# Kernel tuning notes

Hardware: AMD Instinct MI355X
Metric: run time of the kernel (lower is better)

The kernel has to match this reference:

```python
import jax, jax.numpy as jnp
import numpy as np

N_NODES = 10000
N_EDGES = 320000
NODE_C = 256
IN_EDGE_C = 256
OUT_EDGE_C = 512
BN_EPS = 1e-5


def setup_inputs() -> dict:
    key = jax.random.key(0)
    ks = jax.random.split(key, 10)
    d_in = 2 * NODE_C + IN_EDGE_C  # 768
    x = jax.random.normal(ks[0], (N_NODES, NODE_C), dtype=jnp.float32)
    edge_index = jax.random.randint(ks[1], (2, N_EDGES), 0, N_NODES, dtype=jnp.int64)
    edge_attr = jax.random.normal(ks[2], (N_EDGES, IN_EDGE_C), dtype=jnp.float32)
    # MLP params (Linear stored as [in, out] for x @ W + b)
    W1 = jax.random.normal(ks[3], (d_in, OUT_EDGE_C), dtype=jnp.float32) / np.sqrt(d_in)
    b1 = jnp.zeros((OUT_EDGE_C,), dtype=jnp.float32)
    W2 = jax.random.normal(ks[4], (OUT_EDGE_C, OUT_EDGE_C), dtype=jnp.float32) / np.sqrt(OUT_EDGE_C)
    b2 = jnp.zeros((OUT_EDGE_C,), dtype=jnp.float32)
    # BatchNorm affine params
    gamma = jnp.ones((OUT_EDGE_C,), dtype=jnp.float32)
    beta = jnp.zeros((OUT_EDGE_C,), dtype=jnp.float32)
    return {"x": x, "edge_index": edge_index, "edge_attr": edge_attr,
            "W1": W1, "b1": b1, "W2": W2, "b2": b2,
            "gamma": gamma, "beta": beta}


def reference(x, edge_index, edge_attr, W1, b1, W2, b2, gamma, beta):
    src = edge_index[0]  # x_j (source / neighbor)
    dst = edge_index[1]  # x_i (target, aggregation index)
    x_i = x[dst]                                  # [E, node_c]
    x_j = x[src]                                  # [E, node_c]
    m = jnp.concatenate([x_i, x_j - x_i, edge_attr], axis=-1)  # [E, 2*node_c+edge_c]
    h = jax.nn.relu(m @ W1 + b1) @ W2 + b2        # per-edge MLP -> [E, out_c]
    out = jax.ops.segment_sum(h, dst, num_segments=x.shape[0])  # scatter-add -> [N, out_c]
    # BatchNorm1d (training-mode batch statistics, biased variance)
    mean = jnp.mean(out, axis=0)
    var = jnp.var(out, axis=0)
    y = (out - mean) * jax.lax.rsqrt(var + BN_EPS) * gamma + beta
    return jax.nn.relu(y)
```

## Files before the change

kernel.cpp:

```cpp
#include <hip/hip_runtime.h>
#include <hip/hip_bf16.h>
#include <cstdint>

#define NN 10000
#define NE 320000
#define NC 256
#define OC 512
#define K1 256

typedef __bf16 bf16_t;
typedef bf16_t bf16x8 __attribute__((ext_vector_type(8)));
typedef bf16_t bf16x4 __attribute__((ext_vector_type(4)));
typedef float  f32x4  __attribute__((ext_vector_type(4)));

__device__ __forceinline__ void gload_lds16(const void* g, void* l) {
  __builtin_amdgcn_global_load_lds(
      (const __attribute__((address_space(1))) unsigned int*)g,
      (__attribute__((address_space(3))) unsigned int*)l, 16, 0, 0);
}

__device__ __forceinline__ int permB(int R) {
  return (R & ~63) + ((R & 15) << 2) + ((R >> 4) & 3);
}

__global__ void k_prep(const float* __restrict__ x,
                       const float* __restrict__ W1,
                       const float* __restrict__ W2,
                       bf16_t* __restrict__ xb,
                       bf16_t* __restrict__ w1abt,
                       bf16_t* __restrict__ w1ct,
                       bf16_t* __restrict__ w2t,
                       float* __restrict__ agg,
                       int* __restrict__ deg,
                       int* __restrict__ cursor,
                       float* __restrict__ sums) {
  const int stride = gridDim.x * blockDim.x;
  for (int i = blockIdx.x * blockDim.x + threadIdx.x; i < NN * OC; i += stride) {
    agg[i] = 0.0f;
    if (i < NN * NC) xb[i] = (bf16_t)x[i];
    if (i < 1024 * K1) {
      const int n = i >> 8, k = i & 255;
      float w;
      if (n < OC) w = W1[(size_t)k * OC + n] - W1[(size_t)(k + NC) * OC + n];
      else        w = W1[(size_t)(k + NC) * OC + (n - OC)];
      w1abt[i] = (bf16_t)w;
    }
    if (i < OC * K1) {
      const int n = i >> 8, k = i & 255;
      w1ct[i] = (bf16_t)W1[(size_t)(512 + k) * OC + n];
    }
    if (i < OC * OC) {
      const int n = i >> 9, k = i & 511;
      w2t[i] = (bf16_t)W2[(size_t)k * OC + n];
    }
    if (i < NN) { deg[i] = 0; cursor[i] = 0; }
    if (i < 1024) sums[i] = 0.0f;
  }
}

__global__ void k_deg(const int* __restrict__ dstIdx, int* __restrict__ deg) {
  const int i = blockIdx.x * blockDim.x + threadIdx.x;
  if (i < NE) atomicAdd(&deg[dstIdx[i]], 1);
}

__global__ void k_scan(const int* __restrict__ deg, int* __restrict__ offs) {
  __shared__ int carry;
  __shared__ int wsum[4];
  if (threadIdx.x == 0) carry = 0;
  __syncthreads();
  const int lane = threadIdx.x & 63, w = threadIdx.x >> 6;
  for (int base = 0; base < NN; base += 256) {
    const int i = base + threadIdx.x;
    const int v = (i < NN) ? deg[i] : 0;
    int s = v;
#pragma unroll
    for (int d = 1; d < 64; d <<= 1) { int t = __shfl_up(s, d); if (lane >= d) s += t; }
    if (lane == 63) wsum[w] = s;
    __syncthreads();
    int woff = 0;
    for (int j = 0; j < w; j++) woff += wsum[j];
    const int incl = s + woff + carry;
    if (i < NN) offs[i] = incl - v;
    __syncthreads();
    if (threadIdx.x == 255) carry = incl;
    __syncthreads();
  }
}

__global__ void k_scatter(const int* __restrict__ srcIdx, const int* __restrict__ dstIdx,
                          const int* __restrict__ offs, int* __restrict__ cursor,
                          int* __restrict__ eperm, int* __restrict__ sdst,
                          int* __restrict__ ssrc) {
  const int e = blockIdx.x * blockDim.x + threadIdx.x;
  if (e < NE) {
    const int d = dstIdx[e];
    const int pos = offs[d] + atomicAdd(&cursor[d], 1);
    eperm[pos] = e;
    sdst[pos] = d;
    ssrc[pos] = srcIdx[e];
  }
}

__global__ __launch_bounds__(256) void k_pq(
    const bf16_t* __restrict__ xb,
    const bf16_t* __restrict__ w1abt,
    const float*  __restrict__ b1,
    float*        __restrict__ P,
    bf16_t*       __restrict__ Qb) {
  __shared__ bf16_t sA[128 * 64];
  __shared__ bf16_t sB[128 * 64];

  const int tid = threadIdx.x;
  const int cb = blockIdx.x & 7, rblk = blockIdx.x >> 3;
  const int r0 = rblk * 128, n0 = cb * 128;
  const int lane = tid & 63, wid = tid >> 6;
  const int mbase = (wid >> 1) * 64, nbase = (wid & 1) * 64;
  const int lr = lane >> 3, ls = lane & 7, slog = ls ^ lr;
  const int g = lane >> 4;

  f32x4 acc[4][4];
#pragma unroll
  for (int mi = 0; mi < 4; mi++)
#pragma unroll
    for (int ni = 0; ni < 4; ni++) acc[mi][ni] = (f32x4){0.f, 0.f, 0.f, 0.f};

  for (int kb = 0; kb < K1; kb += 64) {
#pragma unroll
    for (int i = 0; i < 4; i++) {
      const int row = wid * 32 + i * 8;
      int grow = r0 + row + lr;
      if (grow > NN - 1) grow = NN - 1;
      gload_lds16(xb + (size_t)grow * NC + kb + slog * 8, &sA[row * 64]);
      gload_lds16(w1abt + (size_t)(n0 + permB(row + lr)) * K1 + kb + slog * 8,
                  &sB[row * 64]);
    }
    __syncthreads();
#pragma unroll
    for (int kk = 0; kk < 2; kk++) {
      const int sl = kk * 4 + g;
      bf16x8 av[4], bv[4];
#pragma unroll
      for (int mi = 0; mi < 4; mi++) {
        const int rA = mbase + mi * 16 + (lane & 15);
        av[mi] = *(const bf16x8*)&sA[rA * 64 + ((sl ^ (rA & 7)) * 8)];
      }
#pragma unroll
      for (int ni = 0; ni < 4; ni++) {
        const int rB = nbase + ni * 16 + (lane & 15);
        bv[ni] = *(const bf16x8*)&sB[rB * 64 + ((sl ^ (rB & 7)) * 8)];
      }
#pragma unroll
      for (int mi = 0; mi < 4; mi++)
#pragma unroll
        for (int ni = 0; ni < 4; ni++)
          acc[mi][ni] = __builtin_amdgcn_mfma_f32_16x16x32_bf16(av[mi], bv[ni], acc[mi][ni], 0, 0, 0);
    }
    __syncthreads();
  }

  const int col0 = n0 + nbase + (lane & 15) * 4;
  f32x4 b1v = {0.f, 0.f, 0.f, 0.f};
  if (col0 < OC) b1v = *(const f32x4*)&b1[col0];
#pragma unroll
  for (int mi = 0; mi < 4; mi++) {
#pragma unroll
    for (int q = 0; q < 4; q++) {
      const int grow = r0 + mbase + mi * 16 + g * 4 + q;
      if (grow < NN) {
        if (col0 < OC) {
          f32x4 v;
#pragma unroll
          for (int j = 0; j < 4; j++) v[j] = acc[mi][j][q] + b1v[j];
          *(f32x4*)&P[(size_t)grow * OC + col0] = v;
        } else {
          bf16x4 v;
#pragma unroll
          for (int j = 0; j < 4; j++) v[j] = (bf16_t)acc[mi][j][q];
          *(bf16x4*)&Qb[(size_t)grow * OC + (col0 - OC)] = v;
        }
      }
    }
  }
}

__global__ __launch_bounds__(256, 2) void k_edge_gemm(
    const float*  __restrict__ ea,
    const bf16_t* __restrict__ w1ct,
    const float*  __restrict__ P,
    const bf16_t* __restrict__ Qb,
    const int*    __restrict__ eperm,
    const int*    __restrict__ sdst,
    const int*    __restrict__ ssrc,
    float*        __restrict__ agg) {
  __shared__ bf16_t sM[2][128 * 64];
  __shared__ bf16_t sW[2][128 * 64];
  __shared__ int sDst[128];
  __shared__ int sSrc[128];
  __shared__ int sE[128];

  const int bid = (blockIdx.x & 7) * 1250 + (blockIdx.x >> 3);
  const int cb = bid & 3, eblk = bid >> 2;
  const int e0 = eblk * 128, n0 = cb * 128;

  const int tid = threadIdx.x;
  if (tid < 128) {
    sDst[tid] = sdst[e0 + tid];
    sSrc[tid] = ssrc[e0 + tid];
    sE[tid]   = eperm[e0 + tid];
  }
  __syncthreads();

  const int lane = tid & 63, wid = tid >> 6;
  const int mbase = (wid >> 1) * 64, nbase = (wid & 1) * 64;
  const int g = lane >> 4, r = lane & 15;
  const int lr = lane >> 3, ls = lane & 7, slogW = ls ^ lr;
  const int mrow = tid >> 1, qd = tid & 1;
  const int msw = mrow & 7;
  const float* eaRow = ea + (size_t)sE[mrow] * NC;

#define STAGE_W(kt, b)                                                        \
  _Pragma("unroll") for (int i = 0; i < 4; i++) {                             \
    const int rowb = wid * 32 + i * 8;                                        \
    gload_lds16(w1ct + (size_t)(n0 + permB(rowb + lr)) * K1 + (kt)*64 + slogW * 8, \
                &sW[b][rowb * 64]);                                           \
  }
#define LOAD_A(kt)                                                            \
  _Pragma("unroll") for (int j = 0; j < 8; j++)                               \
      a[j] = *(const f32x4*)(eaRow + (kt)*64 + qd * 32 + j * 4);
#define WRITE_M(b)                                                            \
  _Pragma("unroll") for (int tt = 0; tt < 4; tt++) {                          \
    const int slot = qd * 4 + tt;                                             \
    bf16x8 v;                                                                 \
    _Pragma("unroll") for (int jj = 0; jj < 4; jj++) {                        \
      v[jj] = (bf16_t)a[tt * 2][jj];                                          \
      v[4 + jj] = (bf16_t)a[tt * 2 + 1][jj];                                  \
    }                                                                         \
    *(bf16x8*)&sM[b][mrow * 64 + ((slot ^ msw) * 8)] = v;                     \
  }

  f32x4 a[8];
  STAGE_W(0, 0);
  LOAD_A(0);

  const int col0 = n0 + nbase + r * 4;
  f32x4  Pp[4][4];
  bf16x4 Qp[4][4];
#pragma unroll
  for (int mi = 0; mi < 4; mi++) {
    const int rbase = mbase + mi * 16 + g * 4;
#pragma unroll
    for (int q = 0; q < 4; q++) {
      Pp[mi][q] = *(const f32x4*)&P[(size_t)sDst[rbase + q] * OC + col0];
      Qp[mi][q] = *(const bf16x4*)&Qb[(size_t)sSrc[rbase + q] * OC + col0];
    }
  }

  WRITE_M(0);

  f32x4 acc[4][4];
#pragma unroll
  for (int mi = 0; mi < 4; mi++)
#pragma unroll
    for (int ni = 0; ni < 4; ni++) acc[mi][ni] = (f32x4){0.f, 0.f, 0.f, 0.f};

#pragma unroll
  for (int t = 0; t < 4; t++) {
    const int b = t & 1;
    __syncthreads();
    if (t < 3) { STAGE_W(t + 1, b ^ 1); LOAD_A(t + 1); }
#pragma unroll
    for (int kk = 0; kk < 2; kk++) {
      const int sl = kk * 4 + g;
      bf16x8 av[4], bv[4];
#pragma unroll
      for (int mi = 0; mi < 4; mi++) {
        const int rA = mbase + mi * 16 + r;
        av[mi] = *(const bf16x8*)&sM[b][rA * 64 + ((sl ^ (rA & 7)) * 8)];
      }
#pragma unroll
      for (int ni = 0; ni < 4; ni++) {
        const int rB = nbase + ni * 16 + r;
        bv[ni] = *(const bf16x8*)&sW[b][rB * 64 + ((sl ^ (rB & 7)) * 8)];
      }
#pragma unroll
      for (int mi = 0; mi < 4; mi++)
#pragma unroll
        for (int ni = 0; ni < 4; ni++)
          acc[mi][ni] = __builtin_amdgcn_mfma_f32_16x16x32_bf16(av[mi], bv[ni], acc[mi][ni], 0, 0, 0);
    }
    if (t < 3) { WRITE_M(b ^ 1); }
  }
#undef STAGE_W
#undef LOAD_A
#undef WRITE_M

#pragma unroll
  for (int mi = 0; mi < 4; mi++) {
    const int rbase = mbase + mi * 16 + g * 4;
    const int d0 = sDst[rbase],     d1 = sDst[rbase + 1];
    const int d2 = sDst[rbase + 2], d3 = sDst[rbase + 3];
    const int headId = d0, tailId = d3;
    const bool b1q = (d1 != d0), b2q = (d2 != d1), b3q = (d3 != d2);
    const bool seen = b1q | b2q | b3q;
    bool match[3];
#pragma unroll
    for (int j = 0; j < 3; j++) {
      const int tIdj = __shfl(tailId, (lane & 15) | (j << 4));
      match[j] = (j < g) && (tIdj == headId);
    }
    const int nextHead = __shfl(headId, (lane + 16) & 63);
    const bool endsHere = (g == 3) || (nextHead != tailId);

    f32x4 v0, v1, v2, v3;
#pragma unroll
    for (int j = 0; j < 4; j++) {
      v0[j] = fmaxf(acc[mi][j][0] + Pp[mi][0][j] + (float)Qp[mi][0][j], 0.f);
      v1[j] = fmaxf(acc[mi][j][1] + Pp[mi][1][j] + (float)Qp[mi][1][j], 0.f);
      v2[j] = fmaxf(acc[mi][j][2] + Pp[mi][2][j] + (float)Qp[mi][2][j], 0.f);
      v3[j] = fmaxf(acc[mi][j][3] + Pp[mi][3][j] + (float)Qp[mi][3][j], 0.f);
    }

    f32x4 head = {0.f, 0.f, 0.f, 0.f}, run = v0;
    bool first = true;
    if (b1q) { head = run; first = false; run = v1; } else run += v1;
    if (b2q) {
      if (first) { head = run; first = false; }
      else {
        float* base = agg + (size_t)d1 * OC + col0;
#pragma unroll
        for (int j = 0; j < 4; j++) if (run[j] != 0.f) atomicAdd(base + j, run[j]);
      }
      run = v2;
    } else run += v2;
    if (b3q) {
      if (first) { head = run; first = false; }
      else {
        float* base = agg + (size_t)d2 * OC + col0;
#pragma unroll
        for (int j = 0; j < 4; j++) if (run[j] != 0.f) atomicAdd(base + j, run[j]);
      }
      run = v3;
    } else run += v3;
    const f32x4 tailSum = run;

    f32x4 inc = {0.f, 0.f, 0.f, 0.f};
#pragma unroll
    for (int jg = 0; jg < 3; jg++) {
      f32x4 ts;
#pragma unroll
      for (int c = 0; c < 4; c++) ts[c] = __shfl(tailSum[c], (lane & 15) | (jg << 4));
      if (match[jg]) inc += ts;
    }
    if (seen) {
      float* base = agg + (size_t)headId * OC + col0;
#pragma unroll
      for (int j = 0; j < 4; j++) {
        const float h = head[j] + inc[j];
        if (h != 0.f) atomicAdd(base + j, h);
      }
    }
    if (endsHere) {
      float* base = agg + (size_t)tailId * OC + col0;
#pragma unroll
      for (int j = 0; j < 4; j++) {
        const float t2 = tailSum[j] + (seen ? 0.f : inc[j]);
        if (t2 != 0.f) atomicAdd(base + j, t2);
      }
    }
  }
}

__global__ __launch_bounds__(256) void k_node_gemm(
    const float*  __restrict__ agg,
    const bf16_t* __restrict__ w2t,
    const float*  __restrict__ b2,
    const int*    __restrict__ deg,
    float*        __restrict__ out,
    float*        __restrict__ sums) {
  __shared__ bf16_t sM[128 * 72];
  __shared__ bf16_t sW[128 * 72];

  const int tid  = threadIdx.x;
  const int bid  = blockIdx.x;
  const int cb   = bid & 3;
  const int rblk = bid >> 2;
  const int r0   = rblk * 128;
  const int n0   = cb * 128;

  const int lane  = tid & 63, wid = tid >> 6;
  const int mbase = (wid >> 1) * 64, nbase = (wid & 1) * 64;
  const int se = tid >> 1;
  const int sk = (tid & 1) * 32;
  const int arow  = r0 + se;
  const bool rowok = arow < NN;

  f32x4 acc[4][4];
#pragma unroll
  for (int mi = 0; mi < 4; mi++)
#pragma unroll
    for (int ni = 0; ni < 4; ni++) acc[mi][ni] = (f32x4){0.f, 0.f, 0.f, 0.f};

  for (int kb = 0; kb < OC; kb += 64) {
    {
      bf16x8* dst = (bf16x8*)&sM[se * 72 + sk];
      if (rowok) {
        const float* pf = agg + (size_t)arow * OC + kb + sk;
        f32x4 f[8];
#pragma unroll
        for (int i = 0; i < 8; i++) f[i] = *(const f32x4*)(pf + i * 4);
#pragma unroll
        for (int i = 0; i < 4; i++) {
          bf16x8 v;
#pragma unroll
          for (int j = 0; j < 4; j++) {
            v[j]     = (bf16_t)f[2 * i][j];
            v[4 + j] = (bf16_t)f[2 * i + 1][j];
          }
          dst[i] = v;
        }
      } else {
        bf16x8 z = {};
        dst[0] = z; dst[1] = z; dst[2] = z; dst[3] = z;
      }
    }
    {
      const bf16_t* pw = w2t + (size_t)(n0 + permB(se)) * OC + kb + sk;
      bf16x8* dst = (bf16x8*)&sW[se * 72 + sk];
      dst[0] = *(const bf16x8*)(pw);
      dst[1] = *(const bf16x8*)(pw + 8);
      dst[2] = *(const bf16x8*)(pw + 16);
      dst[3] = *(const bf16x8*)(pw + 24);
    }
    __syncthreads();
#pragma unroll
    for (int kk = 0; kk < 2; kk++) {
      const int krd = kk * 32 + (lane >> 4) * 8;
      bf16x8 av[4], bv[4];
#pragma unroll
      for (int mi = 0; mi < 4; mi++)
        av[mi] = *(const bf16x8*)&sM[(mbase + mi * 16 + (lane & 15)) * 72 + krd];
#pragma unroll
      for (int ni = 0; ni < 4; ni++)
        bv[ni] = *(const bf16x8*)&sW[(nbase + ni * 16 + (lane & 15)) * 72 + krd];
#pragma unroll
      for (int mi = 0; mi < 4; mi++)
#pragma unroll
        for (int ni = 0; ni < 4; ni++)
          acc[mi][ni] = __builtin_amdgcn_mfma_f32_16x16x32_bf16(av[mi], bv[ni], acc[mi][ni], 0, 0, 0);
    }
    __syncthreads();
  }

  const int col0 = n0 + nbase + (lane & 15) * 4;
  const f32x4 b2v = *(const f32x4*)&b2[col0];
  const int g = lane >> 4;
  f32x4 s1 = {0.f, 0.f, 0.f, 0.f}, s2 = {0.f, 0.f, 0.f, 0.f};
#pragma unroll
  for (int mi = 0; mi < 4; mi++) {
#pragma unroll
    for (int q = 0; q < 4; q++) {
      const int row = r0 + mbase + mi * 16 + g * 4 + q;
      if (row < NN) {
        const float dg = (float)deg[row];
        f32x4 v;
#pragma unroll
        for (int j = 0; j < 4; j++) {
          v[j] = acc[mi][j][q] + b2v[j] * dg;
          s1[j] += v[j];
          s2[j] += v[j] * v[j];
        }
        *(f32x4*)&out[(size_t)row * OC + col0] = v;
      }
    }
  }
#pragma unroll
  for (int j = 0; j < 4; j++) {
    s1[j] += __shfl_xor(s1[j], 16);  s2[j] += __shfl_xor(s2[j], 16);
    s1[j] += __shfl_xor(s1[j], 32);  s2[j] += __shfl_xor(s2[j], 32);
  }
  if (g == 0) {
#pragma unroll
    for (int j = 0; j < 4; j++) {
      atomicAdd(&sums[col0 + j], s1[j]);
      atomicAdd(&sums[OC + col0 + j], s2[j]);
    }
  }
}

__global__ void k_bn_apply(float* __restrict__ out,
                           const float* __restrict__ sums,
                           const float* __restrict__ gamma,
                           const float* __restrict__ beta) {
  const int i = blockIdx.x * blockDim.x + threadIdx.x;
  f32x4 v = *((const f32x4*)out + i);
  const int c = (i & 127) << 2;
  const f32x4 sm = *(const f32x4*)&sums[c];
  const f32x4 sq = *(const f32x4*)&sums[OC + c];
  const f32x4 gm = *(const f32x4*)&gamma[c];
  const f32x4 bt = *(const f32x4*)&beta[c];
  f32x4 r;
#pragma unroll
  for (int j = 0; j < 4; j++) {
    const float mean = sm[j] * (1.0f / NN);
    const float var  = sq[j] * (1.0f / NN) - mean * mean;
    const float sc   = rsqrtf(var + 1e-5f) * gm[j];
    r[j] = fmaxf(v[j] * sc + (bt[j] - mean * sc), 0.0f);
  }
  *((f32x4*)out + i) = r;
}

extern "C" void kernel_launch(void* const* d_in, const int* in_sizes, int n_in,
                              void* d_out, int out_size, void* d_ws, size_t ws_size,
                              hipStream_t stream) {
  const float* x     = (const float*)d_in[0];
  const int*   ei    = (const int*)d_in[1];
  const float* ea    = (const float*)d_in[2];
  const float* W1    = (const float*)d_in[3];
  const float* b1    = (const float*)d_in[4];
  const float* W2    = (const float*)d_in[5];
  const float* b2    = (const float*)d_in[6];
  const float* gamma = (const float*)d_in[7];
  const float* beta  = (const float*)d_in[8];
  float* out = (float*)d_out;

  char* ws = (char*)d_ws;
  float*  agg    = (float*)(ws);
  float*  P      = (float*)(ws + 20480000);
  bf16_t* Qb     = (bf16_t*)(ws + 40960000);
  bf16_t* xb     = (bf16_t*)(ws + 51200000);
  bf16_t* w1abt  = (bf16_t*)(ws + 56320000);
  bf16_t* w1ct   = (bf16_t*)(ws + 56844288);
  bf16_t* w2t    = (bf16_t*)(ws + 57106432);
  int*    deg    = (int*)(ws + 57630720);
  int*    offs   = (int*)(ws + 57670720);
  int*    cursor = (int*)(ws + 57710720);
  float*  sums   = (float*)(ws + 57750720);
  int*    eperm  = (int*)(ws + 57754816);
  int*    sdst   = (int*)(ws + 59034816);
  int*    ssrc   = (int*)(ws + 60314816);

  const int* srcIdx = ei;
  const int* dstIdx = ei + NE;

  k_prep<<<4096, 256, 0, stream>>>(x, W1, W2, xb, w1abt, w1ct, w2t, agg, deg, cursor, sums);
  k_deg<<<(NE + 255) / 256, 256, 0, stream>>>(dstIdx, deg);
  k_scan<<<1, 256, 0, stream>>>(deg, offs);
  k_scatter<<<(NE + 255) / 256, 256, 0, stream>>>(srcIdx, dstIdx, offs, cursor,
                                                  eperm, sdst, ssrc);
  k_pq<<<((NN + 127) / 128) * 8, 256, 0, stream>>>(xb, w1abt, b1, P, Qb);
  k_edge_gemm<<<(NE / 128) * 4, 256, 0, stream>>>(ea, w1ct, P, Qb, eperm, sdst, ssrc, agg);
  k_node_gemm<<<((NN + 127) / 128) * 4, 256, 0, stream>>>(agg, w2t, b2, deg, out, sums);
  k_bn_apply<<<(NN * OC / 4 + 255) / 256, 256, 0, stream>>>(out, sums, gamma, beta);
}
```

Baseline: 500.3 us.

## Split edge GEMM block into eight waves with narrower column tiles

The edge GEMM block grows from 256 to 512 threads, and each wave now covers a 64x32 output tile instead of 64x64. The ea-row staging and W-tile loads are redistributed across the extra threads, using a new column permutation that matches the two-column-per-lane epilogue. The P/Q gathers move from before the K loop into the epilogue, which cuts accumulator and prefetch register pressure so more waves can be resident. In exchange, the gather latency is no longer hidden behind the MFMA loop, and the loads become narrower 8-byte/4-byte accesses.

```diff
diff --git a/kernel.cpp b/kernel.cpp
--- a/kernel.cpp
+++ b/kernel.cpp
@@ -11,7 +11,9 @@
 typedef __bf16 bf16_t;
 typedef bf16_t bf16x8 __attribute__((ext_vector_type(8)));
 typedef bf16_t bf16x4 __attribute__((ext_vector_type(4)));
+typedef bf16_t bf16x2 __attribute__((ext_vector_type(2)));
 typedef float  f32x4  __attribute__((ext_vector_type(4)));
+typedef float  f32x2  __attribute__((ext_vector_type(2)));
 
 __device__ __forceinline__ void gload_lds16(const void* g, void* l) {
   __builtin_amdgcn_global_load_lds(
@@ -21,6 +23,9 @@
 
 __device__ __forceinline__ int permB(int R) {
   return (R & ~63) + ((R & 15) << 2) + ((R >> 4) & 3);
+}
+__device__ __forceinline__ int permB32(int R) {
+  return (R & ~31) + ((R & 15) << 1) + ((R >> 4) & 1);
 }
 
 __global__ void k_prep(const float* __restrict__ x,
@@ -183,7 +188,7 @@
   }
 }
 
-__global__ __launch_bounds__(256, 2) void k_edge_gemm(
+__global__ __launch_bounds__(512, 4) void k_edge_gemm(
     const float*  __restrict__ ea,
     const bf16_t* __restrict__ w1ct,
     const float*  __restrict__ P,
@@ -211,25 +216,26 @@
   __syncthreads();
 
   const int lane = tid & 63, wid = tid >> 6;
-  const int mbase = (wid >> 1) * 64, nbase = (wid & 1) * 64;
+  const int mbase = (wid >> 2) * 64;
+  const int nbase = (wid & 3) * 32;
   const int g = lane >> 4, r = lane & 15;
   const int lr = lane >> 3, ls = lane & 7, slogW = ls ^ lr;
-  const int mrow = tid >> 1, qd = tid & 1;
+  const int mrow = tid >> 2, qd = tid & 3;
   const int msw = mrow & 7;
   const float* eaRow = ea + (size_t)sE[mrow] * NC;
 
 #define STAGE_W(kt, b)                                                        \
-  _Pragma("unroll") for (int i = 0; i < 4; i++) {                             \
-    const int rowb = wid * 32 + i * 8;                                        \
-    gload_lds16(w1ct + (size_t)(n0 + permB(rowb + lr)) * K1 + (kt)*64 + slogW * 8, \
+  _Pragma("unroll") for (int i = 0; i < 2; i++) {                             \
+    const int rowb = wid * 16 + i * 8;       \
+    gload_lds16(w1ct + (size_t)(n0 + permB32(rowb + lr)) * K1 + (kt)*64 + slogW * 8, \
                 &sW[b][rowb * 64]);                                           \
   }
 #define LOAD_A(kt)                                                            \
-  _Pragma("unroll") for (int j = 0; j < 8; j++)                               \
-      a[j] = *(const f32x4*)(eaRow + (kt)*64 + qd * 32 + j * 4);
+  _Pragma("unroll") for (int j = 0; j < 4; j++)                               \
+      a[j] = *(const f32x4*)(eaRow + (kt)*64 + qd * 16 + j * 4);
 #define WRITE_M(b)                                                            \
-  _Pragma("unroll") for (int tt = 0; tt < 4; tt++) {                          \
-    const int slot = qd * 4 + tt;                                             \
+  _Pragma("unroll") for (int tt = 0; tt < 2; tt++) {                          \
+    const int slot = qd * 2 + tt;                                             \
     bf16x8 v;                                                                 \
     _Pragma("unroll") for (int jj = 0; jj < 4; jj++) {                        \
       v[jj] = (bf16_t)a[tt * 2][jj];                                          \
@@ -238,30 +244,16 @@
     *(bf16x8*)&sM[b][mrow * 64 + ((slot ^ msw) * 8)] = v;                     \
   }
 
-  f32x4 a[8];
+  f32x4 a[4];
   STAGE_W(0, 0);
   LOAD_A(0);
-
-  const int col0 = n0 + nbase + r * 4;
-  f32x4  Pp[4][4];
-  bf16x4 Qp[4][4];
-#pragma unroll
-  for (int mi = 0; mi < 4; mi++) {
-    const int rbase = mbase + mi * 16 + g * 4;
-#pragma unroll
-    for (int q = 0; q < 4; q++) {
-      Pp[mi][q] = *(const f32x4*)&P[(size_t)sDst[rbase + q] * OC + col0];
-      Qp[mi][q] = *(const bf16x4*)&Qb[(size_t)sSrc[rbase + q] * OC + col0];
-    }
-  }
-
   WRITE_M(0);
 
-  f32x4 acc[4][4];
+  f32x4 acc[4][2];
 #pragma unroll
   for (int mi = 0; mi < 4; mi++)
 #pragma unroll
-    for (int ni = 0; ni < 4; ni++) acc[mi][ni] = (f32x4){0.f, 0.f, 0.f, 0.f};
+    for (int ni = 0; ni < 2; ni++) acc[mi][ni] = (f32x4){0.f, 0.f, 0.f, 0.f};
 
 #pragma unroll
   for (int t = 0; t < 4; t++) {
@@ -271,21 +263,21 @@
 #pragma unroll
     for (int kk = 0; kk < 2; kk++) {
       const int sl = kk * 4 + g;
-      bf16x8 av[4], bv[4];
+      bf16x8 av[4], bv[2];
 #pragma unroll
       for (int mi = 0; mi < 4; mi++) {
         const int rA = mbase + mi * 16 + r;
         av[mi] = *(const bf16x8*)&sM[b][rA * 64 + ((sl ^ (rA & 7)) * 8)];
       }
 #pragma unroll
-      for (int ni = 0; ni < 4; ni++) {
+      for (int ni = 0; ni < 2; ni++) {
         const int rB = nbase + ni * 16 + r;
         bv[ni] = *(const bf16x8*)&sW[b][rB * 64 + ((sl ^ (rB & 7)) * 8)];
       }
 #pragma unroll
       for (int mi = 0; mi < 4; mi++)
 #pragma unroll
-        for (int ni = 0; ni < 4; ni++)
+        for (int ni = 0; ni < 2; ni++)
           acc[mi][ni] = __builtin_amdgcn_mfma_f32_16x16x32_bf16(av[mi], bv[ni], acc[mi][ni], 0, 0, 0);
     }
     if (t < 3) { WRITE_M(b ^ 1); }
@@ -294,11 +286,14 @@
 #undef LOAD_A
 #undef WRITE_M
 
+  const int col0 = n0 + nbase + r * 2;
 #pragma unroll
   for (int mi = 0; mi < 4; mi++) {
     const int rbase = mbase + mi * 16 + g * 4;
     const int d0 = sDst[rbase],     d1 = sDst[rbase + 1];
     const int d2 = sDst[rbase + 2], d3 = sDst[rbase + 3];
+    const int s0 = sSrc[rbase],     s1 = sSrc[rbase + 1];
+    const int s2 = sSrc[rbase + 2], s3 = sSrc[rbase + 3];
     const int headId = d0, tailId = d3;
     const bool b1q = (d1 != d0), b2q = (d2 != d1), b3q = (d3 != d2);
     const bool seen = b1q | b2q | b3q;
@@ -311,16 +306,25 @@
     const int nextHead = __shfl(headId, (lane + 16) & 63);
     const bool endsHere = (g == 3) || (nextHead != tailId);
 
-    f32x4 v0, v1, v2, v3;
-#pragma unroll
-    for (int j = 0; j < 4; j++) {
-      v0[j] = fmaxf(acc[mi][j][0] + Pp[mi][0][j] + (float)Qp[mi][0][j], 0.f);
-      v1[j] = fmaxf(acc[mi][j][1] + Pp[mi][1][j] + (float)Qp[mi][1][j], 0.f);
-      v2[j] = fmaxf(acc[mi][j][2] + Pp[mi][2][j] + (float)Qp[mi][2][j], 0.f);
-      v3[j] = fmaxf(acc[mi][j][3] + Pp[mi][3][j] + (float)Qp[mi][3][j], 0.f);
-    }
-
-    f32x4 head = {0.f, 0.f, 0.f, 0.f}, run = v0;
+    const f32x2 P0 = *(const f32x2*)&P[(size_t)d0 * OC + col0];
+    const f32x2 P1 = *(const f32x2*)&P[(size_t)d1 * OC + col0];
+    const f32x2 P2 = *(const f32x2*)&P[(size_t)d2 * OC + col0];
+    const f32x2 P3 = *(const f32x2*)&P[(size_t)d3 * OC + col0];
+    const bf16x2 Q0 = *(const bf16x2*)&Qb[(size_t)s0 * OC + col0];
+    const bf16x2 Q1 = *(const bf16x2*)&Qb[(size_t)s1 * OC + col0];
+    const bf16x2 Q2 = *(const bf16x2*)&Qb[(size_t)s2 * OC + col0];
+    const bf16x2 Q3 = *(const bf16x2*)&Qb[(size_t)s3 * OC + col0];
+
+    f32x2 v0, v1, v2, v3;
+#pragma unroll
+    for (int j = 0; j < 2; j++) {
+      v0[j] = fmaxf(acc[mi][j][0] + P0[j] + (float)Q0[j], 0.f);
+      v1[j] = fmaxf(acc[mi][j][1] + P1[j] + (float)Q1[j], 0.f);
+      v2[j] = fmaxf(acc[mi][j][2] + P2[j] + (float)Q2[j], 0.f);
+      v3[j] = fmaxf(acc[mi][j][3] + P3[j] + (float)Q3[j], 0.f);
+    }
+
+    f32x2 head = {0.f, 0.f}, run = v0;
     bool first = true;
     if (b1q) { head = run; first = false; run = v1; } else run += v1;
     if (b2q) {
@@ -328,7 +332,7 @@
       else {
         float* base = agg + (size_t)d1 * OC + col0;
 #pragma unroll
-        for (int j = 0; j < 4; j++) if (run[j] != 0.f) atomicAdd(base + j, run[j]);
+        for (int j = 0; j < 2; j++) if (run[j] != 0.f) atomicAdd(base + j, run[j]);
       }
       run = v2;
     } else run += v2;
@@ -337,24 +341,24 @@
       else {
         float* base = agg + (size_t)d2 * OC + col0;
 #pragma unroll
-        for (int j = 0; j < 4; j++) if (run[j] != 0.f) atomicAdd(base + j, run[j]);
+        for (int j = 0; j < 2; j++) if (run[j] != 0.f) atomicAdd(base + j, run[j]);
       }
       run = v3;
     } else run += v3;
-    const f32x4 tailSum = run;
-
-    f32x4 inc = {0.f, 0.f, 0.f, 0.f};
+    const f32x2 tailSum = run;
+
+    f32x2 inc = {0.f, 0.f};
 #pragma unroll
     for (int jg = 0; jg < 3; jg++) {
-      f32x4 ts;
-#pragma unroll
-      for (int c = 0; c < 4; c++) ts[c] = __shfl(tailSum[c], (lane & 15) | (jg << 4));
+      f32x2 ts;
+#pragma unroll
+      for (int c = 0; c < 2; c++) ts[c] = __shfl(tailSum[c], (lane & 15) | (jg << 4));
       if (match[jg]) inc += ts;
     }
     if (seen) {
       float* base = agg + (size_t)headId * OC + col0;
 #pragma unroll
-      for (int j = 0; j < 4; j++) {
+      for (int j = 0; j < 2; j++) {
         const float h = head[j] + inc[j];
         if (h != 0.f) atomicAdd(base + j, h);
       }
@@ -362,7 +366,7 @@
     if (endsHere) {
       float* base = agg + (size_t)tailId * OC + col0;
 #pragma unroll
-      for (int j = 0; j < 4; j++) {
+      for (int j = 0; j < 2; j++) {
         const float t2 = tailSum[j] + (seen ? 0.f : inc[j]);
         if (t2 != 0.f) atomicAdd(base + j, t2);
       }
@@ -548,7 +552,7 @@
   k_scatter<<<(NE + 255) / 256, 256, 0, stream>>>(srcIdx, dstIdx, offs, cursor,
                                                   eperm, sdst, ssrc);
   k_pq<<<((NN + 127) / 128) * 8, 256, 0, stream>>>(xb, w1abt, b1, P, Qb);
-  k_edge_gemm<<<(NE / 128) * 4, 256, 0, stream>>>(ea, w1ct, P, Qb, eperm, sdst, ssrc, agg);
+  k_edge_gemm<<<(NE / 128) * 4, 512, 0, stream>>>(ea, w1ct, P, Qb, eperm, sdst, ssrc, agg);
   k_node_gemm<<<((NN + 127) / 128) * 4, 256, 0, stream>>>(agg, w2t, b2, deg, out, sums);
   k_bn_apply<<<(NN * OC / 4 + 255) / 256, 256, 0, stream>>>(out, sums, gamma, beta);
 }
```

Result: faster. 424.8 us (median of 2 runs) (-15.1%).
